# Performance work log

Hardware: AMD Instinct MI355X
Metric: run time of the kernel (lower is better)

Reference implementation:

```python
import jax, jax.numpy as jnp
import numpy as np

KH = KW = 3
PAD = 1
STRIDE = 1
H_OUT = W_OUT = 32  # (32 - 3 + 2)/1 + 1


def unfold2d(X):
    # torch.nn.functional.unfold ordering: feature index = c*KH*KW + i*KW + j
    B, C, H, W = X.shape
    Xp = jnp.pad(X, ((0, 0), (0, 0), (PAD, PAD), (PAD, PAD)))
    patches = [Xp[:, :, i:i + H_OUT * STRIDE:STRIDE, j:j + W_OUT * STRIDE:STRIDE]
               for i in range(KH) for j in range(KW)]
    u = jnp.stack(patches, axis=2)            # (B, C, KH*KW, H_out, W_out)
    return u.reshape(B, C * KH * KW, H_OUT * W_OUT)  # (B, K, S)


def setup_inputs() -> dict:
    key = jax.random.key(0)
    k1, k2, k3 = jax.random.split(key, 3)
    B, C_in, C_out = 64, 128, 64
    S = H_OUT * W_OUT           # 1024 spatial locations
    K = C_in * KH * KW          # 1152 unfolded features
    # xavier-uniform-ish scale for per-location weights
    lim = float(np.sqrt(6.0 / (K + C_out)))
    X = jax.random.normal(k1, (B, C_in, 32, 32), dtype=jnp.float32)
    weight = jax.random.uniform(k2, (S, K, C_out), minval=-lim, maxval=lim, dtype=jnp.float32)
    bias = jax.random.uniform(k3, (H_OUT, W_OUT), minval=-0.3, maxval=0.3, dtype=jnp.float32)
    return {"X": X, "weight": weight, "bias": bias}


def reference(X, weight, bias):
    B = X.shape[0]
    C_out = weight.shape[-1]
    ufld = unfold2d(X)                          # (B, K, S)
    ufld = ufld + bias.reshape(1, 1, -1)        # per-location bias added to unfolded values
    h = jnp.einsum('bks,skc->bcs', ufld, weight)  # per-location batched GEMM
    return h.reshape(B, C_out, H_OUT, W_OUT)
```

## Files before the change

### kernel.cpp

```cpp
#include <hip/hip_runtime.h>

typedef short v8s __attribute__((ext_vector_type(8)));
typedef float v4f __attribute__((ext_vector_type(4)));

__device__ __forceinline__ unsigned rne_hi(float f) {
    unsigned u = __float_as_uint(f);
    return u + 0x7FFFu + ((u >> 16) & 1u);
}

__global__ __launch_bounds__(256) void xpose_kernel(const float* __restrict__ X,
                                                    unsigned short* __restrict__ Xt) {
    __shared__ float tile[64][65];
    const int bx  = blockIdx.x;
    const int c   = bx >> 4;
    const int hw0 = (bx & 15) << 6;
    const int t    = threadIdx.x;
    const int lane = t & 63;
    const int brow = t >> 6;

#pragma unroll
    for (int r = 0; r < 16; ++r) {
        int b = brow + (r << 2);
        tile[b][lane] = X[((size_t)(b * 128 + c) << 10) + hw0 + lane];
    }
    __syncthreads();
#pragma unroll
    for (int r = 0; r < 16; ++r) {
        int row = brow + (r << 2);
        float f = tile[lane][row];
        Xt[(((size_t)c << 10) + hw0 + row << 6) + lane] =
            (unsigned short)(rne_hi(f) >> 16);
    }
}

__global__ __launch_bounds__(256, 4) void vconv_kernel(
    const float* __restrict__ Wg,
    const float* __restrict__ bias,
    const unsigned short* __restrict__ Xt,
    float* __restrict__ out)
{
    __shared__ __align__(16) unsigned A_lds[64 * 16];
    __shared__ __align__(16) unsigned B_lds[64 * 16];
    __shared__ int tab[1152];
    __shared__ float csum[16][64];
    __shared__ float csum_tot[64];

    const int s = blockIdx.x;
    const int y = s >> 5, x = s & 31;
    const int t    = threadIdx.x;
    const int lane = t & 63;
    const int wv   = t >> 6;

    for (int k = t; k < 1152; k += 256) {
        int c  = k / 9;
        int r  = k - c * 9;
        int di = r / 3, dj = r - di * 3;
        int yy = y + di - 1, xx = x + dj - 1;
        int off = (((c << 10) + (yy << 5) + xx) << 7);
        bool ok = (yy >= 0) && (yy < 32) && (xx >= 0) && (xx < 32);
        tab[k] = ok ? off : -1;
    }

    const float bias_s = bias[s];

    const int g16 = t & 15;
    const int hi4 = t >> 4;
    const int r4  = g16 << 2;

    const float* wbase = Wg + ((size_t)s * 1152 + (hi4 << 1)) * 64 + r4;

    unsigned waddr[4];
#pragma unroll
    for (int i = 0; i < 4; ++i) {
        int row = r4 + i;
        unsigned grp = (unsigned)((hi4 >> 2) ^ ((row >> 2) & 3));
        waddr[i] = (unsigned)(row << 4) + (grp << 2) + (unsigned)(hi4 & 3);
    }

    const int quad = lane >> 4;
    const int mrow = (wv << 4) + (lane & 15);
    const unsigned a_raddr = (unsigned)(mrow << 4) + ((unsigned)(quad ^ ((mrow >> 2) & 3)) << 2);
    unsigned b_raddr[4];
#pragma unroll
    for (int t0 = 0; t0 < 4; ++t0) {
        int n = (t0 << 4) + (lane & 15);
        b_raddr[t0] = (unsigned)(n << 4) + ((unsigned)(quad ^ ((n >> 2) & 3)) << 2);
    }

    v4f acc[4];
#pragma unroll
    for (int t0 = 0; t0 < 4; ++t0) acc[t0] = (v4f){0.f, 0.f, 0.f, 0.f};
    float cs0 = 0.f, cs1 = 0.f, cs2 = 0.f, cs3 = 0.f;

    __syncthreads();

    for (int kk = 0; kk < 36; ++kk) {
        const float4 F0 = *(const float4*)(wbase + (size_t)kk * 2048);
        const float4 F1 = *(const float4*)(wbase + (size_t)kk * 2048 + 64);

        int k0 = (kk << 5) + (hi4 << 1);
        int o0 = tab[k0];
        int o1 = tab[k0 + 1];
        const char* xb = (const char*)Xt + (r4 << 1);
        uint2 P = *(const uint2*)(xb + (o0 >= 0 ? o0 : 0));
        uint2 Q = *(const uint2*)(xb + (o1 >= 0 ? o1 : 0));
        unsigned m0 = o0 >= 0 ? 0xFFFFFFFFu : 0u;
        unsigned m1 = o1 >= 0 ? 0xFFFFFFFFu : 0u;
        P.x &= m0; P.y &= m0; Q.x &= m1; Q.y &= m1;

        __syncthreads();

        B_lds[waddr[0]] = (rne_hi(F0.x) >> 16) | (rne_hi(F1.x) & 0xFFFF0000u);
        B_lds[waddr[1]] = (rne_hi(F0.y) >> 16) | (rne_hi(F1.y) & 0xFFFF0000u);
        B_lds[waddr[2]] = (rne_hi(F0.z) >> 16) | (rne_hi(F1.z) & 0xFFFF0000u);
        B_lds[waddr[3]] = (rne_hi(F0.w) >> 16) | (rne_hi(F1.w) & 0xFFFF0000u);
        cs0 += F0.x + F1.x;
        cs1 += F0.y + F1.y;
        cs2 += F0.z + F1.z;
        cs3 += F0.w + F1.w;

        A_lds[waddr[0]] = (P.x & 0xFFFFu) | (Q.x << 16);
        A_lds[waddr[1]] = (P.x >> 16)     | (Q.x & 0xFFFF0000u);
        A_lds[waddr[2]] = (P.y & 0xFFFFu) | (Q.y << 16);
        A_lds[waddr[3]] = (P.y >> 16)     | (Q.y & 0xFFFF0000u);

        __syncthreads();

        v8s a = *(const v8s*)&A_lds[a_raddr];
        v8s b0 = *(const v8s*)&B_lds[b_raddr[0]];
        v8s b1 = *(const v8s*)&B_lds[b_raddr[1]];
        v8s b2 = *(const v8s*)&B_lds[b_raddr[2]];
        v8s b3 = *(const v8s*)&B_lds[b_raddr[3]];
        acc[0] = __builtin_amdgcn_mfma_f32_16x16x32_bf16(a, b0, acc[0], 0, 0, 0);
        acc[1] = __builtin_amdgcn_mfma_f32_16x16x32_bf16(a, b1, acc[1], 0, 0, 0);
        acc[2] = __builtin_amdgcn_mfma_f32_16x16x32_bf16(a, b2, acc[2], 0, 0, 0);
        acc[3] = __builtin_amdgcn_mfma_f32_16x16x32_bf16(a, b3, acc[3], 0, 0, 0);
    }

    csum[hi4][r4 + 0] = cs0;
    csum[hi4][r4 + 1] = cs1;
    csum[hi4][r4 + 2] = cs2;
    csum[hi4][r4 + 3] = cs3;
    __syncthreads();
    if (t < 64) {
        float tot = 0.f;
#pragma unroll
        for (int p = 0; p < 16; ++p) tot += csum[p][t];
        csum_tot[t] = tot;
    }
    __syncthreads();

#pragma unroll
    for (int t0 = 0; t0 < 4; ++t0) {
        int n = (t0 << 4) + (lane & 15);
        float cb = bias_s * csum_tot[n];
#pragma unroll
        for (int r = 0; r < 4; ++r) {
            int b = (wv << 4) + (quad << 2) + r;
            out[((size_t)(b * 64 + n) << 10) + s] = acc[t0][r] + cb;
        }
    }
}

extern "C" void kernel_launch(void* const* d_in, const int* in_sizes, int n_in,
                              void* d_out, int out_size, void* d_ws, size_t ws_size,
                              hipStream_t stream) {
    const float* X    = (const float*)d_in[0];
    const float* Wg   = (const float*)d_in[1];
    const float* bias = (const float*)d_in[2];
    float* out = (float*)d_out;
    unsigned short* Xt = (unsigned short*)d_ws;

    xpose_kernel<<<2048, 256, 0, stream>>>(X, Xt);
    vconv_kernel<<<1024, 256, 0, stream>>>(Wg, bias, Xt, out);
}
```

Before: 486.6 us.

## Prefetch next K-tile, 2x2 MFMA warp tiling, stage output through scratch transpose

Restructures the per-location GEMM loop to process two K-slices per iteration with register prefetch of the next slice, double LDS buffers, and raw barriers with explicit lgkm waits. Warps now use a 2x2 MFMA tile, and packed bf16 conversion and perm instructions replace the manual rounding and packing. Out-of-bounds patch reads point at a zeroed pad region, removing the masking. Output is written contiguously to scratch and transposed by a new kernel, which trades strided global stores for an extra kernel and an extra round trip of the output.

```diff
diff --git a/kernel.cpp b/kernel.cpp
--- a/kernel.cpp
+++ b/kernel.cpp
@@ -6,6 +6,30 @@
 __device__ __forceinline__ unsigned rne_hi(float f) {
     unsigned u = __float_as_uint(f);
     return u + 0x7FFFu + ((u >> 16) & 1u);
+}
+
+#if defined(__has_builtin)
+#if __has_builtin(__builtin_amdgcn_cvt_pk_bf16_f32)
+#define HAVE_PK_BF16 1
+#endif
+#endif
+
+__device__ __forceinline__ unsigned pk_bf16(float lo, float hi) {
+#ifdef HAVE_PK_BF16
+    auto r = __builtin_amdgcn_cvt_pk_bf16_f32(lo, hi);
+    unsigned u;
+    __builtin_memcpy(&u, &r, 4);
+    return u;
+#else
+    return (rne_hi(lo) >> 16) | (rne_hi(hi) & 0xFFFF0000u);
+#endif
+}
+
+__device__ __forceinline__ void barrier_raw() {
+    asm volatile("s_barrier" ::: "memory");
+}
+__device__ __forceinline__ void barrier_lgkm() {
+    asm volatile("s_waitcnt lgkmcnt(0)\n\ts_barrier" ::: "memory");
 }
 
 __global__ __launch_bounds__(256) void xpose_kernel(const float* __restrict__ X,
@@ -18,6 +42,8 @@
     const int lane = t & 63;
     const int brow = t >> 6;
 
+    if (bx == 0 && t < 128) Xt[8388608 + t] = 0;
+
 #pragma unroll
     for (int r = 0; r < 16; ++r) {
         int b = brow + (r << 2);
@@ -28,7 +54,7 @@
     for (int r = 0; r < 16; ++r) {
         int row = brow + (r << 2);
         float f = tile[lane][row];
-        Xt[(((size_t)c << 10) + hw0 + row << 6) + lane] =
+        Xt[((((size_t)c << 10) + hw0 + row) << 6) + lane] =
             (unsigned short)(rne_hi(f) >> 16);
     }
 }
@@ -37,12 +63,12 @@
     const float* __restrict__ Wg,
     const float* __restrict__ bias,
     const unsigned short* __restrict__ Xt,
-    float* __restrict__ out)
+    float* __restrict__ scratch)
 {
-    __shared__ __align__(16) unsigned A_lds[64 * 16];
-    __shared__ __align__(16) unsigned B_lds[64 * 16];
+    __shared__ __align__(16) unsigned A_lds[2][1024];
+    __shared__ __align__(16) unsigned B_lds[2][1024];
     __shared__ int tab[1152];
-    __shared__ float csum[16][64];
+    __shared__ float csum[16][65];
     __shared__ float csum_tot[64];
 
     const int s = blockIdx.x;
@@ -50,15 +76,16 @@
     const int t    = threadIdx.x;
     const int lane = t & 63;
     const int wv   = t >> 6;
+    const int mh   = wv >> 1, nh = wv & 1;
 
     for (int k = t; k < 1152; k += 256) {
         int c  = k / 9;
         int r  = k - c * 9;
         int di = r / 3, dj = r - di * 3;
         int yy = y + di - 1, xx = x + dj - 1;
-        int off = (((c << 10) + (yy << 5) + xx) << 7);
+        int off = ((c << 10) + (yy << 5) + xx) << 7;
         bool ok = (yy >= 0) && (yy < 32) && (xx >= 0) && (xx < 32);
-        tab[k] = ok ? off : -1;
+        tab[k] = ok ? off : 16777216;
     }
 
     const float bias_s = bias[s];
@@ -68,6 +95,7 @@
     const int r4  = g16 << 2;
 
     const float* wbase = Wg + ((size_t)s * 1152 + (hi4 << 1)) * 64 + r4;
+    const char*  xb    = (const char*)Xt + (r4 << 1);
 
     unsigned waddr[4];
 #pragma unroll
@@ -77,88 +105,133 @@
         waddr[i] = (unsigned)(row << 4) + (grp << 2) + (unsigned)(hi4 & 3);
     }
 
-    const int quad = lane >> 4;
-    const int mrow = (wv << 4) + (lane & 15);
-    const unsigned a_raddr = (unsigned)(mrow << 4) + ((unsigned)(quad ^ ((mrow >> 2) & 3)) << 2);
-    unsigned b_raddr[4];
-#pragma unroll
-    for (int t0 = 0; t0 < 4; ++t0) {
-        int n = (t0 << 4) + (lane & 15);
-        b_raddr[t0] = (unsigned)(n << 4) + ((unsigned)(quad ^ ((n >> 2) & 3)) << 2);
-    }
-
-    v4f acc[4];
-#pragma unroll
-    for (int t0 = 0; t0 < 4; ++t0) acc[t0] = (v4f){0.f, 0.f, 0.f, 0.f};
+    const int quad = lane >> 4, l15 = lane & 15;
+    unsigned a_raddr[2], b_raddr[2];
+#pragma unroll
+    for (int i = 0; i < 2; ++i) {
+        int ra = (((mh << 1) + i) << 4) + l15;
+        a_raddr[i] = (unsigned)(ra << 4) + ((unsigned)(quad ^ ((ra >> 2) & 3)) << 2);
+        int rb = (((nh << 1) + i) << 4) + l15;
+        b_raddr[i] = (unsigned)(rb << 4) + ((unsigned)(quad ^ ((rb >> 2) & 3)) << 2);
+    }
+
+    v4f acc[2][2];
+#pragma unroll
+    for (int i = 0; i < 2; ++i)
+#pragma unroll
+        for (int j = 0; j < 2; ++j) acc[i][j] = (v4f){0.f, 0.f, 0.f, 0.f};
     float cs0 = 0.f, cs1 = 0.f, cs2 = 0.f, cs3 = 0.f;
 
-    __syncthreads();
-
-    for (int kk = 0; kk < 36; ++kk) {
-        const float4 F0 = *(const float4*)(wbase + (size_t)kk * 2048);
-        const float4 F1 = *(const float4*)(wbase + (size_t)kk * 2048 + 64);
-
-        int k0 = (kk << 5) + (hi4 << 1);
-        int o0 = tab[k0];
-        int o1 = tab[k0 + 1];
-        const char* xb = (const char*)Xt + (r4 << 1);
-        uint2 P = *(const uint2*)(xb + (o0 >= 0 ? o0 : 0));
-        uint2 Q = *(const uint2*)(xb + (o1 >= 0 ? o1 : 0));
-        unsigned m0 = o0 >= 0 ? 0xFFFFFFFFu : 0u;
-        unsigned m1 = o1 >= 0 ? 0xFFFFFFFFu : 0u;
-        P.x &= m0; P.y &= m0; Q.x &= m1; Q.y &= m1;
-
-        __syncthreads();
-
-        B_lds[waddr[0]] = (rne_hi(F0.x) >> 16) | (rne_hi(F1.x) & 0xFFFF0000u);
-        B_lds[waddr[1]] = (rne_hi(F0.y) >> 16) | (rne_hi(F1.y) & 0xFFFF0000u);
-        B_lds[waddr[2]] = (rne_hi(F0.z) >> 16) | (rne_hi(F1.z) & 0xFFFF0000u);
-        B_lds[waddr[3]] = (rne_hi(F0.w) >> 16) | (rne_hi(F1.w) & 0xFFFF0000u);
-        cs0 += F0.x + F1.x;
-        cs1 += F0.y + F1.y;
-        cs2 += F0.z + F1.z;
-        cs3 += F0.w + F1.w;
-
-        A_lds[waddr[0]] = (P.x & 0xFFFFu) | (Q.x << 16);
-        A_lds[waddr[1]] = (P.x >> 16)     | (Q.x & 0xFFFF0000u);
-        A_lds[waddr[2]] = (P.y & 0xFFFFu) | (Q.y << 16);
-        A_lds[waddr[3]] = (P.y >> 16)     | (Q.y & 0xFFFF0000u);
-
-        __syncthreads();
-
-        v8s a = *(const v8s*)&A_lds[a_raddr];
-        v8s b0 = *(const v8s*)&B_lds[b_raddr[0]];
-        v8s b1 = *(const v8s*)&B_lds[b_raddr[1]];
-        v8s b2 = *(const v8s*)&B_lds[b_raddr[2]];
-        v8s b3 = *(const v8s*)&B_lds[b_raddr[3]];
-        acc[0] = __builtin_amdgcn_mfma_f32_16x16x32_bf16(a, b0, acc[0], 0, 0, 0);
-        acc[1] = __builtin_amdgcn_mfma_f32_16x16x32_bf16(a, b1, acc[1], 0, 0, 0);
-        acc[2] = __builtin_amdgcn_mfma_f32_16x16x32_bf16(a, b2, acc[2], 0, 0, 0);
-        acc[3] = __builtin_amdgcn_mfma_f32_16x16x32_bf16(a, b3, acc[3], 0, 0, 0);
+    barrier_lgkm();
+
+    float4 Fa0, Fb0, Fa1, Fb1;
+    uint2  P0, Q0, P1, Q1;
+
+    auto LOAD = [&](int kk2) {
+        const float* wb = wbase + (size_t)kk2 * 4096;
+        Fa0 = *(const float4*)(wb);
+        Fb0 = *(const float4*)(wb + 64);
+        Fa1 = *(const float4*)(wb + 2048);
+        Fb1 = *(const float4*)(wb + 2112);
+        int kb  = (kk2 << 6) + (hi4 << 1);
+        int o00 = tab[kb], o01 = tab[kb + 1];
+        int o10 = tab[kb + 32], o11 = tab[kb + 33];
+        P0 = *(const uint2*)(xb + o00);
+        Q0 = *(const uint2*)(xb + o01);
+        P1 = *(const uint2*)(xb + o10);
+        Q1 = *(const uint2*)(xb + o11);
+    };
+
+    LOAD(0);
+
+    for (int kk = 0; kk < 18; ++kk) {
+        barrier_raw();
+
+        B_lds[0][waddr[0]] = pk_bf16(Fa0.x, Fb0.x);
+        B_lds[0][waddr[1]] = pk_bf16(Fa0.y, Fb0.y);
+        B_lds[0][waddr[2]] = pk_bf16(Fa0.z, Fb0.z);
+        B_lds[0][waddr[3]] = pk_bf16(Fa0.w, Fb0.w);
+        A_lds[0][waddr[0]] = __builtin_amdgcn_perm(Q0.x, P0.x, 0x05040100u);
+        A_lds[0][waddr[1]] = __builtin_amdgcn_perm(Q0.x, P0.x, 0x07060302u);
+        A_lds[0][waddr[2]] = __builtin_amdgcn_perm(Q0.y, P0.y, 0x05040100u);
+        A_lds[0][waddr[3]] = __builtin_amdgcn_perm(Q0.y, P0.y, 0x07060302u);
+        B_lds[1][waddr[0]] = pk_bf16(Fa1.x, Fb1.x);
+        B_lds[1][waddr[1]] = pk_bf16(Fa1.y, Fb1.y);
+        B_lds[1][waddr[2]] = pk_bf16(Fa1.z, Fb1.z);
+        B_lds[1][waddr[3]] = pk_bf16(Fa1.w, Fb1.w);
+        A_lds[1][waddr[0]] = __builtin_amdgcn_perm(Q1.x, P1.x, 0x05040100u);
+        A_lds[1][waddr[1]] = __builtin_amdgcn_perm(Q1.x, P1.x, 0x07060302u);
+        A_lds[1][waddr[2]] = __builtin_amdgcn_perm(Q1.y, P1.y, 0x05040100u);
+        A_lds[1][waddr[3]] = __builtin_amdgcn_perm(Q1.y, P1.y, 0x07060302u);
+
+        cs0 += (Fa0.x + Fb0.x) + (Fa1.x + Fb1.x);
+        cs1 += (Fa0.y + Fb0.y) + (Fa1.y + Fb1.y);
+        cs2 += (Fa0.z + Fb0.z) + (Fa1.z + Fb1.z);
+        cs3 += (Fa0.w + Fb0.w) + (Fa1.w + Fb1.w);
+
+        if (kk < 17) LOAD(kk + 1);
+
+        barrier_lgkm();
+
+#pragma unroll
+        for (int h = 0; h < 2; ++h) {
+            v8s a0 = *(const v8s*)&A_lds[h][a_raddr[0]];
+            v8s a1 = *(const v8s*)&A_lds[h][a_raddr[1]];
+            v8s b0 = *(const v8s*)&B_lds[h][b_raddr[0]];
+            v8s b1 = *(const v8s*)&B_lds[h][b_raddr[1]];
+            acc[0][0] = __builtin_amdgcn_mfma_f32_16x16x32_bf16(a0, b0, acc[0][0], 0, 0, 0);
+            acc[0][1] = __builtin_amdgcn_mfma_f32_16x16x32_bf16(a0, b1, acc[0][1], 0, 0, 0);
+            acc[1][0] = __builtin_amdgcn_mfma_f32_16x16x32_bf16(a1, b0, acc[1][0], 0, 0, 0);
+            acc[1][1] = __builtin_amdgcn_mfma_f32_16x16x32_bf16(a1, b1, acc[1][1], 0, 0, 0);
+        }
     }
 
     csum[hi4][r4 + 0] = cs0;
     csum[hi4][r4 + 1] = cs1;
     csum[hi4][r4 + 2] = cs2;
     csum[hi4][r4 + 3] = cs3;
-    __syncthreads();
+    barrier_lgkm();
     if (t < 64) {
         float tot = 0.f;
 #pragma unroll
         for (int p = 0; p < 16; ++p) tot += csum[p][t];
         csum_tot[t] = tot;
     }
+    barrier_lgkm();
+
+    float* sb = scratch + ((size_t)s << 12);
+#pragma unroll
+    for (int j = 0; j < 2; ++j) {
+        int n = (((nh << 1) + j) << 4) + l15;
+        float cb = bias_s * csum_tot[n];
+#pragma unroll
+        for (int i = 0; i < 2; ++i) {
+#pragma unroll
+            for (int r = 0; r < 4; ++r) {
+                int m = (((mh << 1) + i) << 4) + (quad << 2) + r;
+                sb[(m << 6) + n] = acc[i][j][r] + cb;
+            }
+        }
+    }
+}
+
+__global__ __launch_bounds__(256) void otrans_kernel(const float* __restrict__ S,
+                                                     float* __restrict__ out) {
+    __shared__ float tile[64][65];
+    const int bx = blockIdx.x;
+    const int m0 = (bx & 63) << 6;
+    const int s0 = (bx >> 6) << 6;
+    const int t = threadIdx.x, lane = t & 63, brow = t >> 6;
+#pragma unroll
+    for (int r = 0; r < 16; ++r) {
+        int row = brow + (r << 2);
+        tile[row][lane] = S[((size_t)(s0 + row) << 12) + m0 + lane];
+    }
     __syncthreads();
-
-#pragma unroll
-    for (int t0 = 0; t0 < 4; ++t0) {
-        int n = (t0 << 4) + (lane & 15);
-        float cb = bias_s * csum_tot[n];
-#pragma unroll
-        for (int r = 0; r < 4; ++r) {
-            int b = (wv << 4) + (quad << 2) + r;
-            out[((size_t)(b * 64 + n) << 10) + s] = acc[t0][r] + cb;
-        }
+#pragma unroll
+    for (int r = 0; r < 16; ++r) {
+        int row = brow + (r << 2);
+        out[((size_t)(m0 + row) << 10) + s0 + lane] = tile[lane][row];
     }
 }
 
@@ -169,8 +242,11 @@
     const float* Wg   = (const float*)d_in[1];
     const float* bias = (const float*)d_in[2];
     float* out = (float*)d_out;
+
     unsigned short* Xt = (unsigned short*)d_ws;
+    float* scratch = (float*)((char*)d_ws + 16777472);
 
     xpose_kernel<<<2048, 256, 0, stream>>>(X, Xt);
-    vconv_kernel<<<1024, 256, 0, stream>>>(Wg, bias, Xt, out);
-}
+    vconv_kernel<<<1024, 256, 0, stream>>>(Wg, bias, Xt, scratch);
+    otrans_kernel<<<1024, 256, 0, stream>>>(scratch, out);
+}
```

Result: faster. 438.6 us (-9.9%).
